# Performance work log

Measured on AMD Instinct MI355X. Metric: run time of the kernel, lower is better.

## Reference

```python
import jax, jax.numpy as jnp
import numpy as np

B, H, W, C = 8, 64, 64, 64
C8 = C // 8

def setup_inputs() -> dict:
    key = jax.random.key(0)
    ks = jax.random.split(key, 5)
    x = jax.random.normal(ks[0], (B, H, W, C), dtype=jnp.float32)
    # 1x1 conv kernels (fan-in scaled) + biases
    wq = jax.random.normal(ks[1], (C, C8), dtype=jnp.float32) / np.sqrt(C)
    wk = jax.random.normal(ks[2], (C, C8), dtype=jnp.float32) / np.sqrt(C)
    wv = jax.random.normal(ks[3], (C, C), dtype=jnp.float32) / np.sqrt(C)
    bq = jnp.zeros((C8,), dtype=jnp.float32)
    bk = jnp.zeros((C8,), dtype=jnp.float32)
    bv = jnp.zeros((C,), dtype=jnp.float32)
    gamma = jax.random.normal(ks[4], (), dtype=jnp.float32)
    return {"x": x, "wq": wq, "bq": bq, "wk": wk, "bk": bk,
            "wv": wv, "bv": bv, "gamma": gamma}

def reference(x, wq, bq, wk, bk, wv, bv, gamma):
    b, h, w, c = x.shape
    n = h * w
    # 1x1 convs == per-pixel linear projections
    q = (jnp.einsum('bhwc,cd->bhwd', x, wq) + bq).reshape(b, n, -1)  # [B,N,C/8]
    k = (jnp.einsum('bhwc,cd->bhwd', x, wk) + bk).reshape(b, n, -1)  # [B,N,C/8]
    v = (jnp.einsum('bhwc,cd->bhwd', x, wv) + bv).reshape(b, n, -1)  # [B,N,C]
    # Unscaled attention: softmax over keys (last axis), no 1/sqrt(d)
    attn = jax.nn.softmax(jnp.einsum('bnd,bmd->bnm', q, k), axis=-1)  # [B,N,N]
    out = jnp.einsum('bnm,bmc->bnc', attn, v).reshape(b, h, w, c)
    return out * gamma + x
```

## Files before the change

kernel.cpp:

```cpp
#include <hip/hip_runtime.h>
#include <hip/hip_bf16.h>


#define BB 8
#define NN 4096
#define CC 64
#define PSTRIDE 72
#define LOG2E 1.44269504088896f

typedef _Float16 f16;
typedef _Float16 half8 __attribute__((ext_vector_type(8)));
typedef _Float16 half4 __attribute__((ext_vector_type(4)));
typedef __fp16 fp16x2 __attribute__((ext_vector_type(2)));
typedef float floatx4 __attribute__((ext_vector_type(4)));

static __device__ inline half4 pack4(float a, float b, float c, float d) {
    fp16x2 lo = __builtin_amdgcn_cvt_pkrtz(a, b);
    fp16x2 hi = __builtin_amdgcn_cvt_pkrtz(c, d);
    unsigned int lou = __builtin_bit_cast(unsigned int, lo);
    unsigned int hiu = __builtin_bit_cast(unsigned int, hi);
    unsigned long long packed = (unsigned long long)lou | ((unsigned long long)hiu << 32);
    return __builtin_bit_cast(half4, packed);
}


__global__ __launch_bounds__(256) void proj_all_kernel(
    const float* __restrict__ x,
    const float* __restrict__ wq, const float* __restrict__ bq,
    const float* __restrict__ wk, const float* __restrict__ bk,
    const float* __restrict__ wv, const float* __restrict__ bv,
    f16* __restrict__ Qh, f16* __restrict__ Kf, f16* __restrict__ Vf,
    float* __restrict__ qn2, float* __restrict__ kn2)
{
    __shared__ alignas(16) f16 Ws[80][PSTRIDE];
    __shared__ float Bs[80];
    __shared__ alignas(16) f16 Vs[64][68];
    __shared__ alignas(16) f16 Ks[64][12];
    const int tid = threadIdx.x;

    for (int i = tid; i < 4096; i += 256) {
        int cin = i >> 6, cout = i & 63;
        Ws[cout][cin] = (f16)wv[i];
    }
    for (int i = tid; i < 512; i += 256) {
        int cin = i >> 3, c = i & 7;
        Ws[64 + c][cin] = (f16)(wq[i] * LOG2E);
        Ws[72 + c][cin] = (f16)wk[i];
    }
    if (tid < 80)
        Bs[tid] = (tid < 64) ? bv[tid]
                : (tid < 72 ? bq[tid - 64] * LOG2E : bk[tid - 72]);
    __syncthreads();

    const int wave = tid >> 6, lane = tid & 63;
    const int quad = lane >> 4, n16 = lane & 15;
    const long pb = (long)blockIdx.x * 64;
    const long p0 = pb + wave * 16;
    const int  b   = (int)(pb >> 12);
    const int  nnb = (int)(pb & 4095);

    half8 ax[2];
#pragma unroll
    for (int kh = 0; kh < 2; ++kh) {
        const float* xp = x + (p0 + n16) * 64 + kh * 32 + quad * 8;
        float4 x1 = *(const float4*)xp;
        float4 x2 = *(const float4*)(xp + 4);
        ax[kh][0] = (f16)x1.x; ax[kh][1] = (f16)x1.y;
        ax[kh][2] = (f16)x1.z; ax[kh][3] = (f16)x1.w;
        ax[kh][4] = (f16)x2.x; ax[kh][5] = (f16)x2.y;
        ax[kh][6] = (f16)x2.z; ax[kh][7] = (f16)x2.w;
    }

#pragma unroll
    for (int ct = 0; ct < 5; ++ct) {
        const int cout = (ct < 4) ? ct * 16 + n16 : 64 + n16;
        const float bias = Bs[cout];
        half8 b0 = *(const half8*)(&Ws[cout][quad * 8]);
        half8 b1 = *(const half8*)(&Ws[cout][32 + quad * 8]);
        floatx4 acc = {bias, bias, bias, bias};
        acc = __builtin_amdgcn_mfma_f32_16x16x32_f16(ax[0], b0, acc, 0, 0, 0);
        acc = __builtin_amdgcn_mfma_f32_16x16x32_f16(ax[1], b1, acc, 0, 0, 0);
        if (ct < 4) {
#pragma unroll
            for (int r = 0; r < 4; ++r)
                Vs[wave * 16 + quad * 4 + r][ct * 16 + n16] = (f16)acc[r];
        } else {
            float n2[4];
#pragma unroll
            for (int r = 0; r < 4; ++r) n2[r] = acc[r] * acc[r];
#pragma unroll
            for (int d = 1; d < 8; d <<= 1)
#pragma unroll
                for (int r = 0; r < 4; ++r) n2[r] += __shfl_xor(n2[r], d, 64);
            if (n16 == 0) {
#pragma unroll
                for (int r = 0; r < 4; ++r) qn2[p0 + quad * 4 + r] = n2[r];
            } else if (n16 == 8) {
#pragma unroll
                for (int r = 0; r < 4; ++r) kn2[p0 + quad * 4 + r] = n2[r];
            }
            if (n16 < 8) {
                f16* dst = Qh + (p0 + quad * 4) * 8 + n16;
#pragma unroll
                for (int r = 0; r < 4; ++r) dst[r * 8] = (f16)acc[r];
            } else {
#pragma unroll
                for (int r = 0; r < 4; ++r)
                    Ks[wave * 16 + quad * 4 + r][n16 - 8] = (f16)acc[r];
            }
        }
    }
    __syncthreads();

#pragma unroll
    for (int u = 0; u < 2; ++u) {
        const int tt = wave * 2 + u;
        const int kb = tt >> 2, ct = tt & 3;
        half8 v;
#pragma unroll
        for (int j = 0; j < 8; ++j)
            v[j] = Vs[kb * 32 + quad * 8 + j][ct * 16 + n16];
        const size_t kbg = (size_t)b * 128 + (nnb >> 5) + kb;
        *(half8*)(Vf + (kbg * 4 + ct) * 512 + lane * 8) = v;
    }
    if (quad < 2) {
        half4 kv;
#pragma unroll
        for (int j = 0; j < 4; ++j)
            kv[j] = Ks[wave * 16 + n16][quad * 4 + j];
        const size_t kbg = (size_t)b * 256 + (nnb >> 4) + wave;
        *(half4*)(Kf + kbg * 128 + lane * 4) = kv;
    }
}

__global__ __launch_bounds__(256) void knorm_max_kernel(
    const float* __restrict__ kn2, float* __restrict__ Mk2)
{
    __shared__ float red[4];
    const int b = blockIdx.x, tid = threadIdx.x;
    float mx = 0.f;
    for (int i = tid; i < NN; i += 256) mx = fmaxf(mx, kn2[(size_t)b * NN + i]);
#pragma unroll
    for (int d = 1; d < 64; d <<= 1) mx = fmaxf(mx, __shfl_xor(mx, d, 64));
    if ((tid & 63) == 0) red[tid >> 6] = mx;
    __syncthreads();
    if (tid == 0) {
        float m = fmaxf(fmaxf(red[0], red[1]), fmaxf(red[2], red[3]));
        Mk2[b] = m;
    }
}

__global__ __launch_bounds__(256, 4) void attn_kernel(
    const f16* __restrict__ Qh, const f16* __restrict__ Kf,
    const f16* __restrict__ Vf,
    const float* __restrict__ qn2, const float* __restrict__ Mk2,
    const float* __restrict__ x, const float* __restrict__ gptr,
    float* __restrict__ out)
{
    __shared__ alignas(16) char smem[24576];
    f16*   Pbuf = (f16*)smem;
    float* Obuf = (float*)smem;
    __shared__ float Ls[4][2][16];

    const int tid  = threadIdx.x;
    const int wave = tid >> 6, lane = tid & 63;
    const int quad = lane >> 4, n16 = lane & 15;
    const int ks = wave;

    const int b  = blockIdx.x & 7;
    const int qt = blockIdx.x >> 3;
    const size_t bN = (size_t)b * NN;

    const float mk2 = Mk2[b];

    half4 bq4[2];
    float mfix[2];
#pragma unroll
    for (int qt2 = 0; qt2 < 2; ++qt2) {
        const int q = qt * 32 + qt2 * 16 + n16;
#pragma unroll
        for (int j = 0; j < 4; ++j) bq4[qt2][j] = (f16)0.f;
        if (quad < 2)
            bq4[qt2] = *(const half4*)(Qh + (bN + q) * 8 + quad * 4);
        mfix[qt2] = __builtin_sqrtf(qn2[bN + q] * mk2) - 12.0f;
    }

    floatx4 oacc[2][4];
#pragma unroll
    for (int qt2 = 0; qt2 < 2; ++qt2)
#pragma unroll
        for (int ct = 0; ct < 4; ++ct) oacc[qt2][ct] = (floatx4){0.f, 0.f, 0.f, 0.f};
    float l_loc[2] = {0.f, 0.f};

    const f16* kfb = Kf + ((size_t)b * 256 + ks * 64) * 128;
    const f16* vfb = Vf + ((size_t)b * 128 + ks * 32) * 2048;
    const floatx4 zero4 = {0.f, 0.f, 0.f, 0.f};
    f16* Pw0 = Pbuf + (wave * 2 + 0) * 16 * PSTRIDE;
    f16* Pw1 = Pbuf + (wave * 2 + 1) * 16 * PSTRIDE;

    for (int it = 0; it < 16; ++it) {
        half4 ak[4];
#pragma unroll
        for (int t = 0; t < 4; ++t)
            ak[t] = *(const half4*)(kfb + (it * 4 + t) * 128 + lane * 4);
        half8 av0[4];
#pragma unroll
        for (int ct = 0; ct < 4; ++ct)
            av0[ct] = *(const half8*)(vfb + ((size_t)(it * 2) * 4 + ct) * 512 + lane * 8);

        floatx4 sf[4];
#pragma unroll
        for (int t = 0; t < 4; ++t)
            sf[t] = __builtin_amdgcn_mfma_f32_16x16x16f16(ak[t], bq4[0], zero4, 0, 0, 0);

        half8 av1[4];
#pragma unroll
        for (int ct = 0; ct < 4; ++ct)
            av1[ct] = *(const half8*)(vfb + ((size_t)(it * 2 + 1) * 4 + ct) * 512 + lane * 8);

#pragma unroll
        for (int qt2 = 0; qt2 < 2; ++qt2) {
            if (qt2 == 1) {
#pragma unroll
                for (int t = 0; t < 4; ++t)
                    sf[t] = __builtin_amdgcn_mfma_f32_16x16x16f16(ak[t], bq4[1], zero4, 0, 0, 0);
            }
            const float mf = mfix[qt2];
            float rs = 0.f;
#pragma unroll
            for (int t = 0; t < 4; ++t)
#pragma unroll
                for (int r = 0; r < 4; ++r) {
                    float pv = __builtin_exp2f(sf[t][r] - mf);
                    sf[t][r] = pv;
                    rs += pv;
                }
            l_loc[qt2] += rs;
            f16* Pw = qt2 ? Pw1 : Pw0;
#pragma unroll
            for (int t = 0; t < 4; ++t) {
                half4 pk = pack4(sf[t][0], sf[t][1], sf[t][2], sf[t][3]);
                *(half4*)(Pw + n16 * PSTRIDE + t * 16 + quad * 4) = pk;
            }
        }
        __asm__ volatile("s_waitcnt lgkmcnt(0)" ::: "memory");

#pragma unroll
        for (int qt2 = 0; qt2 < 2; ++qt2) {
            f16* Pw = qt2 ? Pw1 : Pw0;
            half8 bp0 = *(const half8*)(Pw + n16 * PSTRIDE + quad * 8);
            half8 bp1 = *(const half8*)(Pw + n16 * PSTRIDE + 32 + quad * 8);
#pragma unroll
            for (int ct = 0; ct < 4; ++ct)
                oacc[qt2][ct] = __builtin_amdgcn_mfma_f32_16x16x32_f16(av0[ct], bp0, oacc[qt2][ct], 0, 0, 0);
#pragma unroll
            for (int ct = 0; ct < 4; ++ct)
                oacc[qt2][ct] = __builtin_amdgcn_mfma_f32_16x16x32_f16(av1[ct], bp1, oacc[qt2][ct], 0, 0, 0);
        }
    }

    float l_run[2];
#pragma unroll
    for (int qt2 = 0; qt2 < 2; ++qt2) {
        float l = l_loc[qt2];
        l += __shfl_xor(l, 16, 64);
        l += __shfl_xor(l, 32, 64);
        l_run[qt2] = l;
    }

    __syncthreads();
    if (ks > 0) {
#pragma unroll
        for (int qt2 = 0; qt2 < 2; ++qt2) {
            if (quad == 0) Ls[ks][qt2][n16] = l_run[qt2];
            float* ob = Obuf + (((ks - 1) * 2 + qt2) * 64 + lane) * 16;
#pragma unroll
            for (int ct = 0; ct < 4; ++ct)
                *(floatx4*)(ob + ct * 4) = oacc[qt2][ct];
        }
    }
    __syncthreads();
    if (ks == 0) {
        const float g = gptr[0];
#pragma unroll
        for (int qt2 = 0; qt2 < 2; ++qt2) {
            float l = l_run[qt2];
            float o[16];
#pragma unroll
            for (int ct = 0; ct < 4; ++ct)
#pragma unroll
                for (int r = 0; r < 4; ++r) o[ct * 4 + r] = oacc[qt2][ct][r];
#pragma unroll
            for (int p = 1; p < 4; ++p) {
                l += Ls[p][qt2][n16];
                const float* ob = Obuf + (((p - 1) * 2 + qt2) * 64 + lane) * 16;
#pragma unroll
                for (int i = 0; i < 16; ++i) o[i] += ob[i];
            }
            const float scale = g / l;
            const int q = qt * 32 + qt2 * 16 + n16;
#pragma unroll
            for (int ct = 0; ct < 4; ++ct) {
                const size_t idx = (bN + q) * CC + ct * 16 + quad * 4;
                float4 xr = *(const float4*)(x + idx);
                float4 res;
                res.x = o[ct * 4 + 0] * scale + xr.x;
                res.y = o[ct * 4 + 1] * scale + xr.y;
                res.z = o[ct * 4 + 2] * scale + xr.z;
                res.w = o[ct * 4 + 3] * scale + xr.w;
                *(float4*)(out + idx) = res;
            }
        }
    }
}

extern "C" void kernel_launch(void* const* d_in, const int* in_sizes, int n_in,
                              void* d_out, int out_size, void* d_ws, size_t ws_size,
                              hipStream_t stream) {
    const float* x     = (const float*)d_in[0];
    const float* wq    = (const float*)d_in[1];
    const float* bq    = (const float*)d_in[2];
    const float* wk    = (const float*)d_in[3];
    const float* bk    = (const float*)d_in[4];
    const float* wv    = (const float*)d_in[5];
    const float* bv    = (const float*)d_in[6];
    const float* gamma = (const float*)d_in[7];
    float* out = (float*)d_out;

    f16* Qh = (f16*)d_ws;
    f16* Kf = Qh + (size_t)BB * NN * 8;
    f16* Vf = Kf + (size_t)BB * 256 * 128;
    float* qn2 = (float*)(Vf + (size_t)BB * 128 * 4 * 512);
    float* kn2 = qn2 + (size_t)BB * NN;
    float* Mk2 = kn2 + (size_t)BB * NN;

    proj_all_kernel<<<512, 256, 0, stream>>>(x, wq, bq, wk, bk, wv, bv,
                                             Qh, Kf, Vf, qn2, kn2);
    knorm_max_kernel<<<BB, 256, 0, stream>>>(kn2, Mk2);
    attn_kernel<<<BB * 128, 256, 0, stream>>>(Qh, Kf, Vf, qn2, Mk2, x, gamma, out);
}
```

Measured before the change: 130.4 us.

## Fuse key-norm max into projection via atomicMax and fold softmax offset into QK MFMA

Removes the separate key-norm max kernel by having each projection block compute a local max and publish it with an atomicMax on the float bits, after a memset clears the slot. Each projection block now processes two pixel groups, so half as many blocks are launched. K is stored with an extra constant-one channel and Q carries the negated stabilizing offset in that slot, so the subtraction before exp2 happens inside the MFMA. K loads become one 16-byte read per block instead of two 8-byte reads. The risks are an extra memset launch, the offset now rounded to fp16 precision, and atomic contention on eight addresses.

```diff
diff --git a/kernel.cpp b/kernel.cpp
--- a/kernel.cpp
+++ b/kernel.cpp
@@ -30,7 +30,7 @@
     const float* __restrict__ wk, const float* __restrict__ bk,
     const float* __restrict__ wv, const float* __restrict__ bv,
     f16* __restrict__ Qh, f16* __restrict__ Kf, f16* __restrict__ Vf,
-    float* __restrict__ qn2, float* __restrict__ kn2)
+    float* __restrict__ qn2, unsigned int* __restrict__ Mk2u)
 {
     __shared__ alignas(16) f16 Ws[80][PSTRIDE];
     __shared__ float Bs[80];
@@ -54,106 +54,100 @@
 
     const int wave = tid >> 6, lane = tid & 63;
     const int quad = lane >> 4, n16 = lane & 15;
-    const long pb = (long)blockIdx.x * 64;
-    const long p0 = pb + wave * 16;
-    const int  b   = (int)(pb >> 12);
-    const int  nnb = (int)(pb & 4095);
-
-    half8 ax[2];
-#pragma unroll
-    for (int kh = 0; kh < 2; ++kh) {
-        const float* xp = x + (p0 + n16) * 64 + kh * 32 + quad * 8;
-        float4 x1 = *(const float4*)xp;
-        float4 x2 = *(const float4*)(xp + 4);
-        ax[kh][0] = (f16)x1.x; ax[kh][1] = (f16)x1.y;
-        ax[kh][2] = (f16)x1.z; ax[kh][3] = (f16)x1.w;
-        ax[kh][4] = (f16)x2.x; ax[kh][5] = (f16)x2.y;
-        ax[kh][6] = (f16)x2.z; ax[kh][7] = (f16)x2.w;
-    }
-
-#pragma unroll
-    for (int ct = 0; ct < 5; ++ct) {
-        const int cout = (ct < 4) ? ct * 16 + n16 : 64 + n16;
-        const float bias = Bs[cout];
-        half8 b0 = *(const half8*)(&Ws[cout][quad * 8]);
-        half8 b1 = *(const half8*)(&Ws[cout][32 + quad * 8]);
-        floatx4 acc = {bias, bias, bias, bias};
-        acc = __builtin_amdgcn_mfma_f32_16x16x32_f16(ax[0], b0, acc, 0, 0, 0);
-        acc = __builtin_amdgcn_mfma_f32_16x16x32_f16(ax[1], b1, acc, 0, 0, 0);
-        if (ct < 4) {
-#pragma unroll
-            for (int r = 0; r < 4; ++r)
-                Vs[wave * 16 + quad * 4 + r][ct * 16 + n16] = (f16)acc[r];
-        } else {
-            float n2[4];
-#pragma unroll
-            for (int r = 0; r < 4; ++r) n2[r] = acc[r] * acc[r];
-#pragma unroll
-            for (int d = 1; d < 8; d <<= 1)
-#pragma unroll
-                for (int r = 0; r < 4; ++r) n2[r] += __shfl_xor(n2[r], d, 64);
-            if (n16 == 0) {
-#pragma unroll
-                for (int r = 0; r < 4; ++r) qn2[p0 + quad * 4 + r] = n2[r];
-            } else if (n16 == 8) {
-#pragma unroll
-                for (int r = 0; r < 4; ++r) kn2[p0 + quad * 4 + r] = n2[r];
-            }
-            if (n16 < 8) {
-                f16* dst = Qh + (p0 + quad * 4) * 8 + n16;
-#pragma unroll
-                for (int r = 0; r < 4; ++r) dst[r * 8] = (f16)acc[r];
+    const long pbB = (long)blockIdx.x * 128;
+    const int  b   = (int)(pbB >> 12);
+
+    for (int pg = 0; pg < 2; ++pg) {
+        const long p0  = pbB + pg * 64 + wave * 16;
+        const int  nnb = (int)((pbB + pg * 64) & 4095);
+
+        half8 ax[2];
+#pragma unroll
+        for (int kh = 0; kh < 2; ++kh) {
+            const float* xp = x + (p0 + n16) * 64 + kh * 32 + quad * 8;
+            float4 x1 = *(const float4*)xp;
+            float4 x2 = *(const float4*)(xp + 4);
+            ax[kh][0] = (f16)x1.x; ax[kh][1] = (f16)x1.y;
+            ax[kh][2] = (f16)x1.z; ax[kh][3] = (f16)x1.w;
+            ax[kh][4] = (f16)x2.x; ax[kh][5] = (f16)x2.y;
+            ax[kh][6] = (f16)x2.z; ax[kh][7] = (f16)x2.w;
+        }
+
+        float kmax = 0.f;
+#pragma unroll
+        for (int ct = 0; ct < 5; ++ct) {
+            const int cout = (ct < 4) ? ct * 16 + n16 : 64 + n16;
+            const float bias = Bs[cout];
+            half8 b0 = *(const half8*)(&Ws[cout][quad * 8]);
+            half8 b1 = *(const half8*)(&Ws[cout][32 + quad * 8]);
+            floatx4 acc = {bias, bias, bias, bias};
+            acc = __builtin_amdgcn_mfma_f32_16x16x32_f16(ax[0], b0, acc, 0, 0, 0);
+            acc = __builtin_amdgcn_mfma_f32_16x16x32_f16(ax[1], b1, acc, 0, 0, 0);
+            if (ct < 4) {
+#pragma unroll
+                for (int r = 0; r < 4; ++r)
+                    Vs[wave * 16 + quad * 4 + r][ct * 16 + n16] = (f16)acc[r];
             } else {
-#pragma unroll
-                for (int r = 0; r < 4; ++r)
-                    Ks[wave * 16 + quad * 4 + r][n16 - 8] = (f16)acc[r];
-            }
-        }
-    }
-    __syncthreads();
-
-#pragma unroll
-    for (int u = 0; u < 2; ++u) {
-        const int tt = wave * 2 + u;
-        const int kb = tt >> 2, ct = tt & 3;
-        half8 v;
-#pragma unroll
-        for (int j = 0; j < 8; ++j)
-            v[j] = Vs[kb * 32 + quad * 8 + j][ct * 16 + n16];
-        const size_t kbg = (size_t)b * 128 + (nnb >> 5) + kb;
-        *(half8*)(Vf + (kbg * 4 + ct) * 512 + lane * 8) = v;
-    }
-    if (quad < 2) {
-        half4 kv;
-#pragma unroll
-        for (int j = 0; j < 4; ++j)
-            kv[j] = Ks[wave * 16 + n16][quad * 4 + j];
-        const size_t kbg = (size_t)b * 256 + (nnb >> 4) + wave;
-        *(half4*)(Kf + kbg * 128 + lane * 4) = kv;
-    }
-}
-
-__global__ __launch_bounds__(256) void knorm_max_kernel(
-    const float* __restrict__ kn2, float* __restrict__ Mk2)
-{
-    __shared__ float red[4];
-    const int b = blockIdx.x, tid = threadIdx.x;
-    float mx = 0.f;
-    for (int i = tid; i < NN; i += 256) mx = fmaxf(mx, kn2[(size_t)b * NN + i]);
-#pragma unroll
-    for (int d = 1; d < 64; d <<= 1) mx = fmaxf(mx, __shfl_xor(mx, d, 64));
-    if ((tid & 63) == 0) red[tid >> 6] = mx;
-    __syncthreads();
-    if (tid == 0) {
-        float m = fmaxf(fmaxf(red[0], red[1]), fmaxf(red[2], red[3]));
-        Mk2[b] = m;
+                float n2[4];
+#pragma unroll
+                for (int r = 0; r < 4; ++r) n2[r] = acc[r] * acc[r];
+#pragma unroll
+                for (int d = 1; d < 8; d <<= 1)
+#pragma unroll
+                    for (int r = 0; r < 4; ++r) n2[r] += __shfl_xor(n2[r], d, 64);
+                if (n16 == 0) {
+#pragma unroll
+                    for (int r = 0; r < 4; ++r) qn2[p0 + quad * 4 + r] = n2[r];
+                } else if (n16 == 8) {
+                    kmax = fmaxf(fmaxf(n2[0], n2[1]), fmaxf(n2[2], n2[3]));
+                }
+                if (n16 < 8) {
+                    f16* dst = Qh + (p0 + quad * 4) * 8 + n16;
+#pragma unroll
+                    for (int r = 0; r < 4; ++r) dst[r * 8] = (f16)acc[r];
+                } else {
+#pragma unroll
+                    for (int r = 0; r < 4; ++r)
+                        Ks[wave * 16 + quad * 4 + r][n16 - 8] = (f16)acc[r];
+                }
+            }
+        }
+        kmax = fmaxf(kmax, __shfl_xor(kmax, 16, 64));
+        kmax = fmaxf(kmax, __shfl_xor(kmax, 32, 64));
+        if (lane == 8) atomicMax(&Mk2u[b], __float_as_uint(kmax));
+        __syncthreads();
+
+#pragma unroll
+        for (int u = 0; u < 2; ++u) {
+            const int tt = wave * 2 + u;
+            const int kb = tt >> 2, ct = tt & 3;
+            half8 v;
+#pragma unroll
+            for (int j = 0; j < 8; ++j)
+                v[j] = Vs[kb * 32 + quad * 8 + j][ct * 16 + n16];
+            const size_t kbg = (size_t)b * 128 + (nnb >> 5) + kb;
+            *(half8*)(Vf + (kbg * 4 + ct) * 512 + lane * 8) = v;
+        }
+        {
+            half4 kv = {0, 0, 0, 0};
+            if (quad < 2) {
+#pragma unroll
+                for (int j = 0; j < 4; ++j)
+                    kv[j] = Ks[wave * 16 + n16][quad * 4 + j];
+            } else if (quad == 2) {
+                kv[0] = (f16)1.f;
+            }
+            const size_t kpg = (size_t)b * 128 + (nnb >> 5) + (wave >> 1);
+            *(half4*)(Kf + kpg * 512 + lane * 8 + (wave & 1) * 4) = kv;
+        }
+        __syncthreads();
     }
 }
 
 __global__ __launch_bounds__(256, 4) void attn_kernel(
     const f16* __restrict__ Qh, const f16* __restrict__ Kf,
     const f16* __restrict__ Vf,
-    const float* __restrict__ qn2, const float* __restrict__ Mk2,
+    const float* __restrict__ qn2, const unsigned int* __restrict__ Mk2u,
     const float* __restrict__ x, const float* __restrict__ gptr,
     float* __restrict__ out)
 {
@@ -171,18 +165,19 @@
     const int qt = blockIdx.x >> 3;
     const size_t bN = (size_t)b * NN;
 
-    const float mk2 = Mk2[b];
+    const float mk2 = __uint_as_float(Mk2u[b]);
 
     half4 bq4[2];
-    float mfix[2];
 #pragma unroll
     for (int qt2 = 0; qt2 < 2; ++qt2) {
         const int q = qt * 32 + qt2 * 16 + n16;
-#pragma unroll
-        for (int j = 0; j < 4; ++j) bq4[qt2][j] = (f16)0.f;
+        const float mf = __builtin_sqrtf(qn2[bN + q] * mk2) - 12.0f;
+        half4 v = {0, 0, 0, 0};
         if (quad < 2)
-            bq4[qt2] = *(const half4*)(Qh + (bN + q) * 8 + quad * 4);
-        mfix[qt2] = __builtin_sqrtf(qn2[bN + q] * mk2) - 12.0f;
+            v = *(const half4*)(Qh + (bN + q) * 8 + quad * 4);
+        else if (quad == 2)
+            v[0] = (f16)(-mf);
+        bq4[qt2] = v;
     }
 
     floatx4 oacc[2][4];
@@ -192,17 +187,21 @@
         for (int ct = 0; ct < 4; ++ct) oacc[qt2][ct] = (floatx4){0.f, 0.f, 0.f, 0.f};
     float l_loc[2] = {0.f, 0.f};
 
-    const f16* kfb = Kf + ((size_t)b * 256 + ks * 64) * 128;
+    const f16* kfb = Kf + ((size_t)b * 128 + ks * 32) * 512;
     const f16* vfb = Vf + ((size_t)b * 128 + ks * 32) * 2048;
     const floatx4 zero4 = {0.f, 0.f, 0.f, 0.f};
     f16* Pw0 = Pbuf + (wave * 2 + 0) * 16 * PSTRIDE;
     f16* Pw1 = Pbuf + (wave * 2 + 1) * 16 * PSTRIDE;
 
     for (int it = 0; it < 16; ++it) {
+        half8 kk0 = *(const half8*)(kfb + (size_t)(it * 2 + 0) * 512 + lane * 8);
+        half8 kk1 = *(const half8*)(kfb + (size_t)(it * 2 + 1) * 512 + lane * 8);
         half4 ak[4];
-#pragma unroll
-        for (int t = 0; t < 4; ++t)
-            ak[t] = *(const half4*)(kfb + (it * 4 + t) * 128 + lane * 4);
+        ak[0] = __builtin_shufflevector(kk0, kk0, 0, 1, 2, 3);
+        ak[1] = __builtin_shufflevector(kk0, kk0, 4, 5, 6, 7);
+        ak[2] = __builtin_shufflevector(kk1, kk1, 0, 1, 2, 3);
+        ak[3] = __builtin_shufflevector(kk1, kk1, 4, 5, 6, 7);
+
         half8 av0[4];
 #pragma unroll
         for (int ct = 0; ct < 4; ++ct)
@@ -225,13 +224,12 @@
                 for (int t = 0; t < 4; ++t)
                     sf[t] = __builtin_amdgcn_mfma_f32_16x16x16f16(ak[t], bq4[1], zero4, 0, 0, 0);
             }
-            const float mf = mfix[qt2];
             float rs = 0.f;
 #pragma unroll
             for (int t = 0; t < 4; ++t)
 #pragma unroll
                 for (int r = 0; r < 4; ++r) {
-                    float pv = __builtin_exp2f(sf[t][r] - mf);
+                    float pv = __builtin_exp2f(sf[t][r]);
                     sf[t][r] = pv;
                     rs += pv;
                 }
@@ -329,13 +327,12 @@
 
     f16* Qh = (f16*)d_ws;
     f16* Kf = Qh + (size_t)BB * NN * 8;
-    f16* Vf = Kf + (size_t)BB * 256 * 128;
+    f16* Vf = Kf + (size_t)BB * 128 * 512;
     float* qn2 = (float*)(Vf + (size_t)BB * 128 * 4 * 512);
-    float* kn2 = qn2 + (size_t)BB * NN;
-    float* Mk2 = kn2 + (size_t)BB * NN;
-
-    proj_all_kernel<<<512, 256, 0, stream>>>(x, wq, bq, wk, bk, wv, bv,
-                                             Qh, Kf, Vf, qn2, kn2);
-    knorm_max_kernel<<<BB, 256, 0, stream>>>(kn2, Mk2);
-    attn_kernel<<<BB * 128, 256, 0, stream>>>(Qh, Kf, Vf, qn2, Mk2, x, gamma, out);
+    unsigned int* Mk2u = (unsigned int*)(qn2 + (size_t)BB * NN);
+
+    hipMemsetAsync(Mk2u, 0, BB * sizeof(unsigned int), stream);
+    proj_all_kernel<<<256, 256, 0, stream>>>(x, wq, bq, wk, bk, wv, bv,
+                                             Qh, Kf, Vf, qn2, Mk2u);
+    attn_kernel<<<BB * 128, 256, 0, stream>>>(Qh, Kf, Vf, qn2, Mk2u, x, gamma, out);
 }
```

After: 149.3 us. +14.5%, slower.
